# Kernel optimization log

Hardware: AMD Instinct MI355X
Metric: run time of the kernel (lower is better)

The kernel has to match this reference:

```python
import jax, jax.numpy as jnp
import numpy as np

B, S, D_IN, D_H = 8, 4096, 1024, 1024

def _uniform(k, shape, bound):
    return jax.random.uniform(k, shape, jnp.float32, -bound, bound)

def setup_inputs() -> dict:
    key = jax.random.key(0)
    ks = jax.random.split(key, 5)
    stdv = 1.0 / np.sqrt(D_IN)
    x = jax.random.normal(ks[0], (B, S, D_IN), jnp.float32)
    Wz = _uniform(ks[1], (D_H, D_IN), stdv)
    bz = _uniform(ks[2], (D_H,), stdv)
    Wh = _uniform(ks[3], (D_H, D_IN), stdv)
    bh = _uniform(ks[4], (D_H,), stdv)
    return {"x": x, "Wz": Wz, "bz": bz, "Wh": Wh, "bh": bh}

def log_g(v):
    # log of g(v) = v+0.5 (v>=0) else sigmoid(v); branch-safe for jit/grad
    return jnp.where(v >= 0, jnp.log(jnp.where(v >= 0, v + 0.5, 1.0)), -jax.nn.softplus(-v))

def reference(x, Wz, bz, Wh, bh):
    # Gate pre-activation k: (B,S,H)
    k = jnp.einsum('bsd,hd->bsh', x, Wz) + bz
    log_z = -jax.nn.softplus(-k)        # log sigmoid(k)
    log_coeffs = -jax.nn.softplus(k)    # log(1 - z)
    pre = jnp.einsum('bsd,hd->bsh', x, Wh) + bh
    log_tilde_h = log_g(pre)
    # h0 = g(0) = 0.5 (default hidden init)
    log_h0 = jnp.full((x.shape[0], 1, Wh.shape[0]), jnp.log(0.5), x.dtype)
    log_b = jnp.concatenate([log_h0, log_z + log_tilde_h], axis=1)  # (B,S+1,H)
    # Heinsen log-space parallel scan: x_t = a_t x_{t-1} + b_t
    a_star = jnp.pad(jnp.cumsum(log_coeffs, axis=1), ((0, 0), (1, 0), (0, 0)))
    log_x = a_star + jax.lax.cumlogsumexp(log_b - a_star, axis=1)
    h = jnp.exp(log_x)
    return h[:, 1:]
```

## Files before the change

### kernel.cpp

```cpp
#include <hip/hip_runtime.h>
#include <cstdint>
#include <cstddef>

#define BB 8
#define SS 4096
#define DI 1024
#define DH 1024
#define MDIM (BB * SS)
#define NC 128
#define CL 32

static constexpr size_t OFF_XB   = 0;
static constexpr size_t OFF_WZB  = 67108864;
static constexpr size_t OFF_WHB  = OFF_WZB + 2097152;
static constexpr size_t OFF_K    = OFF_WHB + 2097152;
static constexpr size_t OFF_P    = OFF_K + 67108864;
static constexpr size_t OFF_CLA  = 0;
static constexpr size_t OFF_CLB  = 4194304;
static constexpr size_t OFF_CAR  = 8388608;

typedef __bf16 bf16;
typedef _Float16 fp16;
typedef short short8 __attribute__((ext_vector_type(8)));
typedef float f4 __attribute__((ext_vector_type(4)));
typedef float f32x8 __attribute__((ext_vector_type(8)));
typedef bf16 bf16x8 __attribute__((ext_vector_type(8)));
typedef fp16 h4 __attribute__((ext_vector_type(4)));

__global__ void convert_kernel(const float* __restrict__ x, const float* __restrict__ wz,
                               const float* __restrict__ wh,
                               bf16* __restrict__ xb, bf16* __restrict__ wzb, bf16* __restrict__ whb) {
    size_t i = ((size_t)blockIdx.x * 256 + threadIdx.x) * 8;
    const float* src; bf16* dst; size_t off;
    if (i < 33554432u) { src = x; dst = xb; off = i; }
    else if (i < 33554432u + 1048576u) { src = wz; dst = wzb; off = i - 33554432u; }
    else { src = wh; dst = whb; off = i - 34603008u; }
    f32x8 v = *(const f32x8*)(src + off);
    bf16x8 o = __builtin_convertvector(v, bf16x8);
    *(bf16x8*)(dst + off) = o;
}

__device__ __forceinline__ void gload_lds16(const void* g, void* l) {
    __builtin_amdgcn_global_load_lds((const __attribute__((address_space(1))) void*)g,
                                     (__attribute__((address_space(3))) void*)l, 16, 0, 0);
}

__device__ __forceinline__ void pbar() {
    asm volatile("" ::: "memory");
    __builtin_amdgcn_s_barrier();
    asm volatile("" ::: "memory");
}

__device__ __forceinline__ void stage_unit(const bf16* __restrict__ src, int row0, char* dst,
                                           int col0 , int w, int l) {
    const int cs = ((l & 3) ^ ((l >> 4) & 2)) << 4;
    const int r = row0 + w * 32 + (l >> 2);
    gload_lds16((const char*)(src + (size_t)r * DI + col0) + cs, dst + w * 2048 + l * 16);
    gload_lds16((const char*)(src + (size_t)(r + 16) * DI + col0) + cs, dst + w * 2048 + 1024 + l * 16);
}

__device__ __forceinline__ void read_a4(short8 (&af)[4], const char* base, int wr, int mf0, int l) {
    const char* p = base + (wr * 128 + mf0 * 16 + (l & 15)) * 64 + (((l >> 4) << 4) ^ ((l & 8) << 2));
#pragma unroll
    for (int i = 0; i < 4; i++) af[i] = *(const short8*)(p + i * 1024);
}

__device__ __forceinline__ void read_b4(short8 (&bf)[4], const char* base, int wc, int l) {
    const char* p = base + (wc * 64 + (l & 15)) * 64 + (((l >> 4) << 4) ^ ((l & 8) << 2));
#pragma unroll
    for (int j = 0; j < 4; j++) bf[j] = *(const short8*)(p + j * 1024);
}

template<int MF0>
__device__ __forceinline__ void mfma16(const short8 (&af)[4], const short8 (&bf)[4], f4 (&acc)[8][4]) {
    __builtin_amdgcn_s_setprio(1);
#pragma unroll
    for (int i = 0; i < 4; i++)
#pragma unroll
        for (int j = 0; j < 4; j++)
            acc[MF0 + i][j] = __builtin_amdgcn_mfma_f32_16x16x32_bf16(af[i], bf[j], acc[MF0 + i][j], 0, 0, 0);
    __builtin_amdgcn_s_setprio(0);
    asm volatile("s_waitcnt lgkmcnt(0)" ::: "memory");
}

template<bool FULL>
__device__ __forceinline__ void ktile_pair(const bf16* __restrict__ A, const bf16* __restrict__ W,
                                           char* lds, int T, int m0, int n0,
                                           int w, int l, int wr, int wc, f4 (&acc)[8][4]) {
    short8 af[4], bf[4];
    read_b4(bf, lds + 32768, wc, l);
    read_a4(af, lds + 0, wr, 0, l);
    stage_unit(A, m0, lds + 81920, (T + 1) * 64 + 32, w, l);
    pbar(); mfma16<0>(af, bf, acc); pbar();
    read_a4(af, lds + 0, wr, 4, l);
    stage_unit(W, n0, lds + 114688, (T + 1) * 64 + 32, w, l);
    pbar(); mfma16<4>(af, bf, acc); pbar();
    read_b4(bf, lds + 49152, wc, l);
    read_a4(af, lds + 16384, wr, 0, l);
    if constexpr (FULL) stage_unit(A, m0, lds + 0, (T + 2) * 64, w, l);
    pbar(); mfma16<0>(af, bf, acc); pbar();
    read_a4(af, lds + 16384, wr, 4, l);
    if constexpr (FULL) {
        stage_unit(W, n0, lds + 32768, (T + 2) * 64, w, l);
        asm volatile("s_waitcnt vmcnt(4)" ::: "memory");
    } else {
        asm volatile("s_waitcnt vmcnt(0)" ::: "memory");
    }
    pbar(); mfma16<4>(af, bf, acc); pbar();
    read_b4(bf, lds + 98304, wc, l);
    read_a4(af, lds + 65536, wr, 0, l);
    if constexpr (FULL) stage_unit(A, m0, lds + 16384, (T + 2) * 64 + 32, w, l);
    pbar(); mfma16<0>(af, bf, acc); pbar();
    read_a4(af, lds + 65536, wr, 4, l);
    if constexpr (FULL) stage_unit(W, n0, lds + 49152, (T + 2) * 64 + 32, w, l);
    pbar(); mfma16<4>(af, bf, acc); pbar();
    read_b4(bf, lds + 114688, wc, l);
    read_a4(af, lds + 81920, wr, 0, l);
    if constexpr (FULL) stage_unit(A, m0, lds + 65536, (T + 3) * 64, w, l);
    pbar(); mfma16<0>(af, bf, acc); pbar();
    read_a4(af, lds + 81920, wr, 4, l);
    if constexpr (FULL) {
        stage_unit(W, n0, lds + 98304, (T + 3) * 64, w, l);
        asm volatile("s_waitcnt vmcnt(4)" ::: "memory");
    } else {
        asm volatile("s_waitcnt vmcnt(0)" ::: "memory");
    }
    pbar(); mfma16<4>(af, bf, acc); pbar();
}

__global__ __launch_bounds__(512, 2)
void gemm256(const bf16* __restrict__ A, const bf16* __restrict__ Wz, const bf16* __restrict__ Wh,
             const float* __restrict__ bz, const float* __restrict__ bh,
             fp16* __restrict__ kout, fp16* __restrict__ pout) {
    __shared__ __attribute__((aligned(16))) char lds[131072];
    const int t = threadIdx.x;
    const int l = t & 63, w = t >> 6;
    const int wr = w >> 2, wc = w & 3;

    const int bid = blockIdx.x;
    const int widx = (bid & 7) * 128 + (bid >> 3);
    const int m_idx = widx >> 3;
    const int gsel = (widx >> 2) & 1;
    const int n_idx = widx & 3;
    const bf16* W = gsel ? Wh : Wz;
    const float* bias = gsel ? bh : bz;
    fp16* out = gsel ? pout : kout;
    const int m0 = m_idx * 256, n0 = n_idx * 256;

    f4 acc[8][4];
#pragma unroll
    for (int i = 0; i < 8; i++)
#pragma unroll
        for (int j = 0; j < 4; j++) acc[i][j] = (f4)(0.f);

    stage_unit(A, m0, lds + 0,     0,  w, l);
    stage_unit(W, n0, lds + 32768, 0,  w, l);
    stage_unit(A, m0, lds + 16384, 32, w, l);
    stage_unit(W, n0, lds + 49152, 32, w, l);
    stage_unit(A, m0, lds + 65536, 64, w, l);
    stage_unit(W, n0, lds + 98304, 64, w, l);
    asm volatile("s_waitcnt vmcnt(4)" ::: "memory");
    pbar();

#pragma unroll 1
    for (int it = 0; it < 7; ++it)
        ktile_pair<true>(A, W, lds, 2 * it, m0, n0, w, l, wr, wc, acc);
    ktile_pair<false>(A, W, lds, 14, m0, n0, w, l, wr, wc, acc);

    const int col16 = l & 15, quad = l >> 4;
#pragma unroll
    for (int nf = 0; nf < 4; nf++) {
        const int cg = n0 + wc * 64 + nf * 16 + col16;
        const float bv = bias[cg];
#pragma unroll
        for (int mf = 0; mf < 8; mf++) {
#pragma unroll
            for (int r = 0; r < 4; r++) {
                const int rg = m0 + wr * 128 + mf * 16 + quad * 4 + r;
                out[(size_t)rg * DH + cg] = (fp16)(acc[mf][nf][r] + bv);
            }
        }
    }
}

__device__ __forceinline__ void gates_lin(float kv, float pv, float& a, float& b) {
    float ek = __expf(-kv);
    float z = __builtin_amdgcn_rcpf(1.f + ek);
    a = 1.f - z;
    float ep = __expf(-pv);
    float gneg = __builtin_amdgcn_rcpf(1.f + ep);
    float g = (pv >= 0.f) ? (pv + 0.5f) : gneg;
    b = z * g;
}

__global__ void scan_pass1(const fp16* __restrict__ kbuf, const fp16* __restrict__ pbuf,
                           float* __restrict__ cla, float* __restrict__ clb) {
    const int tid = blockIdx.x * 256 + threadIdx.x;
    const int hq = tid & 255;
    const int c = (tid >> 8) & 127;
    const int b = tid >> 15;
    size_t base = ((size_t)b * SS + (size_t)c * CL) * DH + hq * 4;

    float A[4] = {1.f, 1.f, 1.f, 1.f};
    float Bc[4] = {0.f, 0.f, 0.f, 0.f};
#pragma unroll 4
    for (int tt = 0; tt < CL; tt++) {
        size_t idx = base + (size_t)tt * DH;
        h4 k4 = *(const h4*)(kbuf + idx);
        h4 p4 = *(const h4*)(pbuf + idx);
#pragma unroll
        for (int q = 0; q < 4; q++) {
            float a, bb;
            gates_lin((float)k4[q], (float)p4[q], a, bb);
            A[q] *= a;
            Bc[q] = fmaf(a, Bc[q], bb);
        }
    }
    const size_t ci = (size_t)(b * NC + c) * DH + hq * 4;
    *(f4*)(cla + ci) = *(f4*)A;
    *(f4*)(clb + ci) = *(f4*)Bc;
}

__global__ void scan_pass2(const float* __restrict__ cla, const float* __restrict__ clb,
                           float* __restrict__ car) {
    const int tid = blockIdx.x * 256 + threadIdx.x;
    const int b = tid >> 10;
    const int h = tid & 1023;
    float carry = 0.5f;
#pragma unroll 8
    for (int c = 0; c < NC; c++) {
        const size_t ci = (size_t)(b * NC + c) * DH + h;
        car[ci] = carry;
        carry = fmaf(cla[ci], carry, clb[ci]);
    }
}

__global__ void scan_pass3(const fp16* __restrict__ kbuf, const fp16* __restrict__ pbuf,
                           const float* __restrict__ car, float* __restrict__ out) {
    const int tid = blockIdx.x * 256 + threadIdx.x;
    const int hq = tid & 255;
    const int c = (tid >> 8) & 127;
    const int b = tid >> 15;
    size_t base = ((size_t)b * SS + (size_t)c * CL) * DH + hq * 4;

    const size_t ci = (size_t)(b * NC + c) * DH + hq * 4;
    f4 car4 = *(const f4*)(car + ci);
    float h[4] = {car4[0], car4[1], car4[2], car4[3]};
#pragma unroll 4
    for (int tt = 0; tt < CL; tt++) {
        size_t idx = base + (size_t)tt * DH;
        h4 k4 = *(const h4*)(kbuf + idx);
        h4 p4 = *(const h4*)(pbuf + idx);
        f4 o;
#pragma unroll
        for (int q = 0; q < 4; q++) {
            float a, bb;
            gates_lin((float)k4[q], (float)p4[q], a, bb);
            h[q] = fmaf(a, h[q], bb);
            o[q] = h[q];
        }
        *(f4*)(out + idx) = o;
    }
}

extern "C" void kernel_launch(void* const* d_in, const int* in_sizes, int n_in,
                              void* d_out, int out_size, void* d_ws, size_t ws_size,
                              hipStream_t stream) {
    const float* x  = (const float*)d_in[0];
    const float* Wz = (const float*)d_in[1];
    const float* bz = (const float*)d_in[2];
    const float* Wh = (const float*)d_in[3];
    const float* bh = (const float*)d_in[4];

    char* ws = (char*)d_ws;
    bf16* xb   = (bf16*)(ws + OFF_XB);
    bf16* wzb  = (bf16*)(ws + OFF_WZB);
    bf16* whb  = (bf16*)(ws + OFF_WHB);
    fp16* kbuf = (fp16*)(ws + OFF_K);
    fp16* pbuf = (fp16*)(ws + OFF_P);
    float* cla  = (float*)(ws + OFF_CLA);
    float* clb  = (float*)(ws + OFF_CLB);
    float* car  = (float*)(ws + OFF_CAR);
    float* out  = (float*)d_out;

    convert_kernel<<<17408, 256, 0, stream>>>(x, Wz, Wh, xb, wzb, whb);

    gemm256<<<1024, 512, 0, stream>>>(xb, wzb, whb, bz, bh, kbuf, pbuf);

    scan_pass1<<<(BB * NC * 256) / 256, 256, 0, stream>>>(kbuf, pbuf, cla, clb);
    scan_pass2<<<(BB * DH) / 256, 256, 0, stream>>>(cla, clb, car);
    scan_pass3<<<(BB * NC * 256) / 256, 256, 0, stream>>>(kbuf, pbuf, car, out);
}
```

Before: 446.2 us.

## Fuse three-pass chunked scan into single kernel with shared-memory chunk scan

Result: slower. 731.0 us (+63.8%).

```diff
diff --git a/kernel.cpp b/kernel.cpp
--- a/kernel.cpp
+++ b/kernel.cpp
@@ -7,17 +7,12 @@
 #define DI 1024
 #define DH 1024
 #define MDIM (BB * SS)
-#define NC 128
-#define CL 32
 
 static constexpr size_t OFF_XB   = 0;
 static constexpr size_t OFF_WZB  = 67108864;
 static constexpr size_t OFF_WHB  = OFF_WZB + 2097152;
 static constexpr size_t OFF_K    = OFF_WHB + 2097152;
 static constexpr size_t OFF_P    = OFF_K + 67108864;
-static constexpr size_t OFF_CLA  = 0;
-static constexpr size_t OFF_CLB  = 4194304;
-static constexpr size_t OFF_CAR  = 8388608;
 
 typedef __bf16 bf16;
 typedef _Float16 fp16;
@@ -193,19 +188,21 @@
     b = z * g;
 }
 
-__global__ void scan_pass1(const fp16* __restrict__ kbuf, const fp16* __restrict__ pbuf,
-                           float* __restrict__ cla, float* __restrict__ clb) {
-    const int tid = blockIdx.x * 256 + threadIdx.x;
-    const int hq = tid & 255;
-    const int c = (tid >> 8) & 127;
-    const int b = tid >> 15;
-    size_t base = ((size_t)b * SS + (size_t)c * CL) * DH + hq * 4;
-
-    float A[4] = {1.f, 1.f, 1.f, 1.f};
-    float Bc[4] = {0.f, 0.f, 0.f, 0.f};
-#pragma unroll 4
-    for (int tt = 0; tt < CL; tt++) {
-        size_t idx = base + (size_t)tt * DH;
+__global__ __launch_bounds__(256, 4)
+void scan_local(const fp16* __restrict__ kbuf, const fp16* __restrict__ pbuf,
+                float* __restrict__ out) {
+    __shared__ f4 sA[2][128][2];
+    __shared__ f4 sB[2][128][2];
+    const int b = blockIdx.x >> 7;
+    const int h0 = (blockIdx.x & 127) * 8;
+    const int c = threadIdx.x >> 1;
+    const int g = threadIdx.x & 1;
+    const size_t base = ((size_t)b * SS + (size_t)c * 32) * DH + h0 + g * 4;
+
+    f4 A = (f4)(1.f), Bc = (f4)(0.f);
+#pragma unroll 8
+    for (int t = 0; t < 32; t++) {
+        size_t idx = base + (size_t)t * DH;
         h4 k4 = *(const h4*)(kbuf + idx);
         h4 p4 = *(const h4*)(pbuf + idx);
 #pragma unroll
@@ -216,39 +213,41 @@
             Bc[q] = fmaf(a, Bc[q], bb);
         }
     }
-    const size_t ci = (size_t)(b * NC + c) * DH + hq * 4;
-    *(f4*)(cla + ci) = *(f4*)A;
-    *(f4*)(clb + ci) = *(f4*)Bc;
-}
-
-__global__ void scan_pass2(const float* __restrict__ cla, const float* __restrict__ clb,
-                           float* __restrict__ car) {
-    const int tid = blockIdx.x * 256 + threadIdx.x;
-    const int b = tid >> 10;
-    const int h = tid & 1023;
-    float carry = 0.5f;
-#pragma unroll 8
-    for (int c = 0; c < NC; c++) {
-        const size_t ci = (size_t)(b * NC + c) * DH + h;
-        car[ci] = carry;
-        carry = fmaf(cla[ci], carry, clb[ci]);
-    }
-}
-
-__global__ void scan_pass3(const fp16* __restrict__ kbuf, const fp16* __restrict__ pbuf,
-                           const float* __restrict__ car, float* __restrict__ out) {
-    const int tid = blockIdx.x * 256 + threadIdx.x;
-    const int hq = tid & 255;
-    const int c = (tid >> 8) & 127;
-    const int b = tid >> 15;
-    size_t base = ((size_t)b * SS + (size_t)c * CL) * DH + hq * 4;
-
-    const size_t ci = (size_t)(b * NC + c) * DH + hq * 4;
-    f4 car4 = *(const f4*)(car + ci);
-    float h[4] = {car4[0], car4[1], car4[2], car4[3]};
+
+    sA[0][c][g] = A;
+    sB[0][c][g] = Bc;
+    __syncthreads();
+    int cur = 0;
+#pragma unroll
+    for (int off = 1; off < 128; off <<= 1) {
+        if (c >= off) {
+            f4 pa = sA[cur][c - off][g];
+            f4 pb = sB[cur][c - off][g];
+#pragma unroll
+            for (int q = 0; q < 4; q++) {
+                Bc[q] = fmaf(A[q], pb[q], Bc[q]);
+                A[q] *= pa[q];
+            }
+        }
+        sA[cur ^ 1][c][g] = A;
+        sB[cur ^ 1][c][g] = Bc;
+        cur ^= 1;
+        __syncthreads();
+    }
+
+    f4 h;
+    if (c == 0) {
+        h = (f4)(0.5f);
+    } else {
+        f4 pa = sA[cur][c - 1][g];
+        f4 pb = sB[cur][c - 1][g];
+#pragma unroll
+        for (int q = 0; q < 4; q++) h[q] = fmaf(pa[q], 0.5f, pb[q]);
+    }
+
 #pragma unroll 4
-    for (int tt = 0; tt < CL; tt++) {
-        size_t idx = base + (size_t)tt * DH;
+    for (int t = 0; t < 32; t++) {
+        size_t idx = base + (size_t)t * DH;
         h4 k4 = *(const h4*)(kbuf + idx);
         h4 p4 = *(const h4*)(pbuf + idx);
         f4 o;
@@ -278,16 +277,11 @@
     bf16* whb  = (bf16*)(ws + OFF_WHB);
     fp16* kbuf = (fp16*)(ws + OFF_K);
     fp16* pbuf = (fp16*)(ws + OFF_P);
-    float* cla  = (float*)(ws + OFF_CLA);
-    float* clb  = (float*)(ws + OFF_CLB);
-    float* car  = (float*)(ws + OFF_CAR);
     float* out  = (float*)d_out;
 
     convert_kernel<<<17408, 256, 0, stream>>>(x, Wz, Wh, xb, wzb, whb);
 
     gemm256<<<1024, 512, 0, stream>>>(xb, wzb, whb, bz, bh, kbuf, pbuf);
 
-    scan_pass1<<<(BB * NC * 256) / 256, 256, 0, stream>>>(kbuf, pbuf, cla, clb);
-    scan_pass2<<<(BB * DH) / 256, 256, 0, stream>>>(cla, clb, car);
-    scan_pass3<<<(BB * NC * 256) / 256, 256, 0, stream>>>(kbuf, pbuf, car, out);
-}
+    scan_local<<<1024, 256, 0, stream>>>(kbuf, pbuf, out);
+}
```
